# Performance work log

Measured on AMD Instinct MI355X. Metric: run time of the kernel, lower is better.

The kernel has to match this reference:

```python
import jax, jax.numpy as jnp
import numpy as np

EMB = 256
HEADS = 8
DH = EMB // HEADS
GRID = (64, 64)
WIN = (8, 8)
B = 16
L = GRID[0] * GRID[1]
LOG100 = float(np.log(100.0))
LN_EPS = 1e-5


def _build_shift_mask():
    # Standard Swin shifted-window attention mask (static, numpy).
    Hh, Ww = GRID; wh, ww = WIN
    sh, sw = wh // 2, ww // 2
    img = np.zeros((Hh, Ww), dtype=np.int32)
    cnt = 0
    for hs in (slice(0, -wh), slice(-wh, -sh), slice(-sh, None)):
        for ws in (slice(0, -ww), slice(-ww, -sw), slice(-sw, None)):
            img[hs, ws] = cnt; cnt += 1
    m = img.reshape(Hh // wh, wh, Ww // ww, ww).transpose(0, 2, 1, 3).reshape(-1, wh * ww)
    mask = np.where(m[:, None, :] != m[:, :, None], -1e4, 0.0).astype(np.float32)
    return jnp.asarray(mask)  # (nWin, N, N)

SHIFT_MASK = _build_shift_mask()


def _layernorm(x, w, b):
    mu = jnp.mean(x, axis=-1, keepdims=True)
    var = jnp.mean(jnp.square(x - mu), axis=-1, keepdims=True)
    return (x - mu) * jax.lax.rsqrt(var + LN_EPS) * w + b


def _window_cos_msa(x, qkv_w, qkv_b, proj_w, proj_b, logit_scale, shifted):
    # x: (B, L, C)
    Hh, Ww = GRID; wh, ww = WIN
    nH, nW = Hh // wh, Ww // ww
    N = wh * ww
    Bb, _, C = x.shape
    xg = x.reshape(Bb, Hh, Ww, C)
    if shifted:
        xg = jnp.roll(xg, (-(wh // 2), -(ww // 2)), axis=(1, 2))
    # window partition -> (B, nWin, N, C)
    xw = xg.reshape(Bb, nH, wh, nW, ww, C).transpose(0, 1, 3, 2, 4, 5).reshape(Bb, nH * nW, N, C)
    qkv = xw @ qkv_w + qkv_b                      # (B, nWin, N, 3C)
    qkv = qkv.reshape(Bb, nH * nW, N, 3, HEADS, DH).transpose(3, 0, 1, 4, 2, 5)
    q, k, v = qkv[0], qkv[1], qkv[2]              # (B, nWin, H, N, DH)
    qn = q / jnp.clip(jnp.linalg.norm(q, axis=-1, keepdims=True), 1e-6)
    kn = k / jnp.clip(jnp.linalg.norm(k, axis=-1, keepdims=True), 1e-6)
    scale = jnp.exp(jnp.minimum(logit_scale, LOG100)).reshape(1, 1, HEADS, 1, 1)
    attn = jnp.einsum('bwhnd,bwhmd->bwhnm', qn, kn) * scale  # cosine attention
    if shifted:
        attn = attn + SHIFT_MASK[None, :, None, :, :]
    attn = jax.nn.softmax(attn, axis=-1)
    out = jnp.einsum('bwhnm,bwhmd->bwhnd', attn, v)          # (B, nWin, H, N, DH)
    out = out.transpose(0, 1, 3, 2, 4).reshape(Bb, nH * nW, N, C)
    out = out @ proj_w + proj_b
    # window merge -> (B, H, W, C)
    out = out.reshape(Bb, nH, nW, wh, ww, C).transpose(0, 1, 3, 2, 4, 5).reshape(Bb, Hh, Ww, C)
    if shifted:
        out = jnp.roll(out, (wh // 2, ww // 2), axis=(1, 2))
    return out.reshape(Bb, Hh * Ww, C)


def _mlp(x, w1, b1, w2, b2):
    h = jax.nn.gelu(x @ w1 + b1, approximate=False)
    return h @ w2 + b2


def setup_inputs() -> dict:
    key = jax.random.key(0)
    ks = jax.random.split(key, 12)
    s = 0.02
    d = {}
    d['x'] = jax.random.normal(ks[0], (B, L, EMB), jnp.float32)
    for i, p in enumerate(('wmsa', 'swmsa')):
        d[p + '_qkv_w'] = jax.random.normal(ks[1 + 3 * i], (EMB, 3 * EMB), jnp.float32) * s
        d[p + '_qkv_b'] = jnp.zeros((3 * EMB,), jnp.float32)
        d[p + '_proj_w'] = jax.random.normal(ks[2 + 3 * i], (EMB, EMB), jnp.float32) * s
        d[p + '_proj_b'] = jnp.zeros((EMB,), jnp.float32)
        d[p + '_logit_scale'] = jnp.full((HEADS,), float(np.log(10.0)), jnp.float32)
    d['ln_w'] = jnp.ones((EMB,), jnp.float32)
    d['ln_b'] = jnp.zeros((EMB,), jnp.float32)
    d['mlp_w1'] = jax.random.normal(ks[7], (EMB, 4 * EMB), jnp.float32) * s
    d['mlp_b1'] = jnp.zeros((4 * EMB,), jnp.float32)
    d['mlp_w2'] = jax.random.normal(ks[8], (4 * EMB, EMB), jnp.float32) * s
    d['mlp_b2'] = jnp.zeros((EMB,), jnp.float32)
    return d


def reference(x, wmsa_qkv_w, wmsa_qkv_b, wmsa_proj_w, wmsa_proj_b, wmsa_logit_scale,
              swmsa_qkv_w, swmsa_qkv_b, swmsa_proj_w, swmsa_proj_b, swmsa_logit_scale,
              ln_w, ln_b, mlp_w1, mlp_b1, mlp_w2, mlp_b2):
    # x = x + LN(WMSA(x)); x = x + LN(MLP(x)); x = x + LN(SWMSA(x)); x = x + LN(MLP(x))
    x = x + _layernorm(_window_cos_msa(x, wmsa_qkv_w, wmsa_qkv_b, wmsa_proj_w, wmsa_proj_b, wmsa_logit_scale, False), ln_w, ln_b)
    x = x + _layernorm(_mlp(x, mlp_w1, mlp_b1, mlp_w2, mlp_b2), ln_w, ln_b)
    x = x + _layernorm(_window_cos_msa(x, swmsa_qkv_w, swmsa_qkv_b, swmsa_proj_w, swmsa_proj_b, swmsa_logit_scale, True), ln_w, ln_b)
    x = x + _layernorm(_mlp(x, mlp_w1, mlp_b1, mlp_w2, mlp_b2), ln_w, ln_b)
    return x
```

## Files before the change

### kernel.cpp

```cpp
#include <hip/hip_runtime.h>
#include <math.h>

typedef __attribute__((ext_vector_type(4))) float f32x4;
typedef __attribute__((ext_vector_type(8))) short bf16x8;

__device__ __forceinline__ short f2bf(float f) {
  unsigned u = __builtin_bit_cast(unsigned, f);
  u += 0x7FFFu + ((u >> 16) & 1u);
  return (short)(u >> 16);
}
__device__ __forceinline__ float bf2f(short s) {
  unsigned u = ((unsigned)(unsigned short)s) << 16;
  return __builtin_bit_cast(float, u);
}

#define MFMA(A, B, C) __builtin_amdgcn_mfma_f32_16x16x32_bf16((A), (B), (C), 0, 0, 0)

#define GLOAD16(gsrc, ldst)                                                      \
  __builtin_amdgcn_global_load_lds(                                              \
      (const __attribute__((address_space(1))) void*)(gsrc),                     \
      (__attribute__((address_space(3))) void*)(ldst), 16, 0, 0)

#define LOG100 4.605170185988092f

__global__ __launch_bounds__(256) void convert_kernel(
    const float* __restrict__ x,
    const float* __restrict__ qw0, const float* __restrict__ qw1,
    const float* __restrict__ pw0, const float* __restrict__ pw1,
    const float* __restrict__ w1, const float* __restrict__ w2,
    short* __restrict__ xb,
    short* __restrict__ qwT0, short* __restrict__ qwT1,
    short* __restrict__ pwT0, short* __restrict__ pwT1,
    short* __restrict__ w1T, short* __restrict__ w2T) {
  int bid = blockIdx.x;
  int tid = threadIdx.x;
  if (bid < 8192) {
    int base = (bid * 256 + tid) * 8;
    bf16x8 o;
#pragma unroll
    for (int j = 0; j < 8; ++j) o[j] = f2bf(x[base + j]);
    *(bf16x8*)&xb[base] = o;
    return;
  }
  int idx = (bid - 8192) * 256 + tid;
  if (idx < 196608) { int n = idx >> 8, k = idx & 255; qwT0[idx] = f2bf(qw0[k * 768 + n]); return; }
  idx -= 196608;
  if (idx < 196608) { int n = idx >> 8, k = idx & 255; qwT1[idx] = f2bf(qw1[k * 768 + n]); return; }
  idx -= 196608;
  if (idx < 65536) { int n = idx >> 8, k = idx & 255; pwT0[idx] = f2bf(pw0[k * 256 + n]); return; }
  idx -= 65536;
  if (idx < 65536) { int n = idx >> 8, k = idx & 255; pwT1[idx] = f2bf(pw1[k * 256 + n]); return; }
  idx -= 65536;
  if (idx < 262144) { int n = idx >> 8, k = idx & 255; w1T[idx] = f2bf(w1[k * 1024 + n]); return; }
  idx -= 262144;
  { int n = idx >> 10, k = idx & 1023; w2T[idx] = f2bf(w2[k * 256 + n]); }
}

template <bool SHIFTED>
__global__ __launch_bounds__(256) void qkv_kernel(
    const short* __restrict__ xb, const short* __restrict__ wT,
    const float* __restrict__ bias,
    short* __restrict__ Q, short* __restrict__ K, short* __restrict__ V,
    int mblk_base) {
  __shared__ short Alds[64][72];
  __shared__ short Blds[256][72];
  const int mloc = blockIdx.x;
  const int mg = mblk_base + mloc;
  const int which = blockIdx.y;
  const int b = mg >> 6, wi = mg & 63;
  const int h0 = (wi >> 3) << 3, w0c = (wi & 7) << 3;
  const int tid = threadIdx.x;
  const int lane = tid & 63, wid = tid >> 6;
  const int l15 = lane & 15, lg = lane >> 4;

  f32x4 zf = {0.f, 0.f, 0.f, 0.f};
  f32x4 acc[4][4];
#pragma unroll
  for (int i = 0; i < 4; ++i)
#pragma unroll
    for (int j = 0; j < 4; ++j) acc[i][j] = zf;

#pragma unroll 1
  for (int kc = 0; kc < 4; ++kc) {
    __syncthreads();
    {
      int c8 = (tid & 7) * 8;
#pragma unroll
      for (int it = 0; it < 2; ++it) {
        int r = (tid >> 3) + it * 32;
        int hs = h0 + (r >> 3), ws2 = w0c + (r & 7);
        if (SHIFTED) { hs = (hs + 4) & 63; ws2 = (ws2 + 4) & 63; }
        int t = b * 4096 + hs * 64 + ws2;
        *(bf16x8*)&Alds[r][c8] = *(const bf16x8*)&xb[t * 256 + kc * 64 + c8];
      }
    }
    {
      int k8 = (tid & 7) * 8;
      int cw = tid >> 3;
#pragma unroll
      for (int p = 0; p < 8; ++p) {
        int col = cw + p * 32;
        *(bf16x8*)&Blds[col][k8] = *(const bf16x8*)&wT[(which * 256 + col) * 256 + kc * 64 + k8];
      }
    }
    __syncthreads();
#pragma unroll
    for (int ks = 0; ks < 2; ++ks) {
      bf16x8 af[4], bfr[4];
#pragma unroll
      for (int ti = 0; ti < 4; ++ti) af[ti] = *(bf16x8*)&Alds[ti * 16 + l15][ks * 32 + lg * 8];
#pragma unroll
      for (int tj = 0; tj < 4; ++tj) bfr[tj] = *(bf16x8*)&Blds[wid * 64 + tj * 16 + l15][ks * 32 + lg * 8];
#pragma unroll
      for (int ti = 0; ti < 4; ++ti)
#pragma unroll
        for (int tj = 0; tj < 4; ++tj) acc[ti][tj] = MFMA(af[ti], bfr[tj], acc[ti][tj]);
    }
  }
  short* outp = (which == 0) ? Q : (which == 1) ? K : V;
#pragma unroll
  for (int tj = 0; tj < 4; ++tj) {
    int c = wid * 64 + tj * 16 + l15;
    int h = c >> 5, d = c & 31;
    float bv = bias[which * 256 + c];
    int hb = (mloc * 8 + h) * 2048;
#pragma unroll
    for (int ti = 0; ti < 4; ++ti) {
#pragma unroll
      for (int idx = 0; idx < 4; ++idx) {
        int n = ti * 16 + lg * 4 + idx;
        float v = acc[ti][tj][idx] + bv;
        int off = hb + (which == 2 ? (d * 64 + n) : (n * 32 + d));
        outp[off] = f2bf(v);
      }
    }
  }
}

template <bool SHIFTED>
__global__ __launch_bounds__(256) void attn_kernel(
    const short* __restrict__ Q, const short* __restrict__ K, const short* __restrict__ V,
    const float* __restrict__ logit_scale,
    const short* __restrict__ projT, const float* __restrict__ proj_b,
    const float* __restrict__ ln_w, const float* __restrict__ ln_b,
    const float* x_old, float* x_new, short* x_new_bf,
    int mblk_base) {
  __shared__ short Plds[4][64][72];
  __shared__ short Olds[64][264];
  __shared__ float red1[4][64], red2[4][64];
  __shared__ int ids[64];

  const int mloc = blockIdx.x;
  const int mg = mblk_base + mloc;
  const int b = mg >> 6, wi = mg & 63;
  const int h0 = (wi >> 3) << 3, w0c = (wi & 7) << 3;
  const int tid = threadIdx.x;
  const int lane = tid & 63, wid = tid >> 6;
  const int l15 = lane & 15, lg = lane >> 4;

  if (SHIFTED) {
    if (tid < 64) {
      int hs = h0 + (tid >> 3), ws2 = w0c + (tid & 7);
      int rr = (hs < 56) ? 0 : ((hs < 60) ? 1 : 2);
      int rc = (ws2 < 56) ? 0 : ((ws2 < 60) ? 1 : 2);
      ids[tid] = rr * 3 + rc;
    }
    __syncthreads();
  }

  f32x4 zf = {0.f, 0.f, 0.f, 0.f};

#pragma unroll 1
  for (int hp = 0; hp < 2; ++hp) {
    const int h = wid * 2 + hp;
    const short* Qh = Q + (mloc * 8 + h) * 2048;
    const short* Kh = K + (mloc * 8 + h) * 2048;
    const short* Vt = V + (mloc * 8 + h) * 2048;
    const float sc = __expf(fminf(logit_scale[h], LOG100));

    bf16x8 qf[4];
#pragma unroll
    for (int ti = 0; ti < 4; ++ti) {
      qf[ti] = *(const bf16x8*)&Qh[(ti * 16 + l15) * 32 + lg * 8];
      float ss = 0.f;
#pragma unroll
      for (int j = 0; j < 8; ++j) { float q = bf2f(qf[ti][j]); ss += q * q; }
      ss += __shfl_xor(ss, 16); ss += __shfl_xor(ss, 32);
      float f = sc / fmaxf(sqrtf(ss), 1e-6f);
#pragma unroll
      for (int j = 0; j < 8; ++j) qf[ti][j] = f2bf(bf2f(qf[ti][j]) * f);
    }
    bf16x8 kf[4];
#pragma unroll
    for (int tj = 0; tj < 4; ++tj) {
      kf[tj] = *(const bf16x8*)&Kh[(tj * 16 + l15) * 32 + lg * 8];
      float ss = 0.f;
#pragma unroll
      for (int j = 0; j < 8; ++j) { float k = bf2f(kf[tj][j]); ss += k * k; }
      ss += __shfl_xor(ss, 16); ss += __shfl_xor(ss, 32);
      float f = 1.f / fmaxf(sqrtf(ss), 1e-6f);
#pragma unroll
      for (int j = 0; j < 8; ++j) kf[tj][j] = f2bf(bf2f(kf[tj][j]) * f);
    }
    f32x4 sacc[4][4];
#pragma unroll
    for (int ti = 0; ti < 4; ++ti)
#pragma unroll
      for (int tj = 0; tj < 4; ++tj) sacc[ti][tj] = MFMA(qf[ti], kf[tj], zf);

    if (SHIFTED) {
      int idc[4];
#pragma unroll
      for (int tj = 0; tj < 4; ++tj) idc[tj] = ids[tj * 16 + l15];
#pragma unroll
      for (int ti = 0; ti < 4; ++ti)
#pragma unroll
        for (int idx = 0; idx < 4; ++idx) {
          int idr = ids[ti * 16 + lg * 4 + idx];
#pragma unroll
          for (int tj = 0; tj < 4; ++tj)
            if (idr != idc[tj]) sacc[ti][tj][idx] += -1e4f;
        }
    }
#pragma unroll
    for (int ti = 0; ti < 4; ++ti) {
#pragma unroll
      for (int idx = 0; idx < 4; ++idx) {
        float m = fmaxf(fmaxf(sacc[ti][0][idx], sacc[ti][1][idx]),
                        fmaxf(sacc[ti][2][idx], sacc[ti][3][idx]));
        m = fmaxf(m, __shfl_xor(m, 1));
        m = fmaxf(m, __shfl_xor(m, 2));
        m = fmaxf(m, __shfl_xor(m, 4));
        m = fmaxf(m, __shfl_xor(m, 8));
        float e0 = __expf(sacc[ti][0][idx] - m);
        float e1 = __expf(sacc[ti][1][idx] - m);
        float e2 = __expf(sacc[ti][2][idx] - m);
        float e3 = __expf(sacc[ti][3][idx] - m);
        float s = e0 + e1 + e2 + e3;
        s += __shfl_xor(s, 1); s += __shfl_xor(s, 2);
        s += __shfl_xor(s, 4); s += __shfl_xor(s, 8);
        float inv = 1.f / s;
        sacc[ti][0][idx] = e0 * inv; sacc[ti][1][idx] = e1 * inv;
        sacc[ti][2][idx] = e2 * inv; sacc[ti][3][idx] = e3 * inv;
      }
    }
#pragma unroll
    for (int ti = 0; ti < 4; ++ti)
#pragma unroll
      for (int tj = 0; tj < 4; ++tj)
#pragma unroll
        for (int idx = 0; idx < 4; ++idx)
          Plds[wid][ti * 16 + lg * 4 + idx][tj * 16 + l15] = f2bf(sacc[ti][tj][idx]);

    f32x4 oacc[4][2];
#pragma unroll
    for (int ti = 0; ti < 4; ++ti)
#pragma unroll
      for (int vj = 0; vj < 2; ++vj) oacc[ti][vj] = zf;
#pragma unroll
    for (int ks = 0; ks < 2; ++ks) {
      bf16x8 pf[4], vf[2];
#pragma unroll
      for (int ti = 0; ti < 4; ++ti) pf[ti] = *(bf16x8*)&Plds[wid][ti * 16 + l15][ks * 32 + lg * 8];
#pragma unroll
      for (int vj = 0; vj < 2; ++vj) vf[vj] = *(const bf16x8*)&Vt[(vj * 16 + l15) * 64 + ks * 32 + lg * 8];
#pragma unroll
      for (int ti = 0; ti < 4; ++ti)
#pragma unroll
        for (int vj = 0; vj < 2; ++vj) oacc[ti][vj] = MFMA(pf[ti], vf[vj], oacc[ti][vj]);
    }
#pragma unroll
    for (int ti = 0; ti < 4; ++ti)
#pragma unroll
      for (int vj = 0; vj < 2; ++vj)
#pragma unroll
        for (int idx = 0; idx < 4; ++idx)
          Olds[ti * 16 + lg * 4 + idx][h * 32 + vj * 16 + l15] = f2bf(oacc[ti][vj][idx]);
  }
  __syncthreads();

  f32x4 pacc[4][4];
#pragma unroll
  for (int i = 0; i < 4; ++i)
#pragma unroll
    for (int j = 0; j < 4; ++j) pacc[i][j] = zf;
#pragma unroll
  for (int kc = 0; kc < 8; ++kc) {
    bf16x8 af[4], bfr[4];
#pragma unroll
    for (int ti = 0; ti < 4; ++ti) af[ti] = *(bf16x8*)&Olds[ti * 16 + l15][kc * 32 + lg * 8];
#pragma unroll
    for (int tj = 0; tj < 4; ++tj)
      bfr[tj] = *(const bf16x8*)&projT[(wid * 64 + tj * 16 + l15) * 256 + kc * 32 + lg * 8];
#pragma unroll
    for (int ti = 0; ti < 4; ++ti)
#pragma unroll
      for (int tj = 0; tj < 4; ++tj) pacc[ti][tj] = MFMA(af[ti], bfr[tj], pacc[ti][tj]);
  }
#pragma unroll
  for (int tj = 0; tj < 4; ++tj) {
    float bv = proj_b[wid * 64 + tj * 16 + l15];
#pragma unroll
    for (int ti = 0; ti < 4; ++ti)
#pragma unroll
      for (int idx = 0; idx < 4; ++idx) pacc[ti][tj][idx] += bv;
  }

#pragma unroll
  for (int ti = 0; ti < 4; ++ti) {
#pragma unroll
    for (int idx = 0; idx < 4; ++idx) {
      float s1 = 0.f, s2 = 0.f;
#pragma unroll
      for (int tj = 0; tj < 4; ++tj) { float v = pacc[ti][tj][idx]; s1 += v; s2 += v * v; }
#pragma unroll
      for (int m = 1; m <= 8; m <<= 1) { s1 += __shfl_xor(s1, m); s2 += __shfl_xor(s2, m); }
      if (l15 == 0) { int row = ti * 16 + lg * 4 + idx; red1[wid][row] = s1; red2[wid][row] = s2; }
    }
  }
  __syncthreads();
#pragma unroll
  for (int ti = 0; ti < 4; ++ti) {
#pragma unroll
    for (int idx = 0; idx < 4; ++idx) {
      int row = ti * 16 + lg * 4 + idx;
      float t1 = red1[0][row] + red1[1][row] + red1[2][row] + red1[3][row];
      float t2 = red2[0][row] + red2[1][row] + red2[2][row] + red2[3][row];
      float mu = t1 * 0.00390625f;
      float var = t2 * 0.00390625f - mu * mu;
      float rstd = rsqrtf(var + 1e-5f);
      int hs = h0 + (row >> 3), ws2 = w0c + (row & 7);
      if (SHIFTED) { hs = (hs + 4) & 63; ws2 = (ws2 + 4) & 63; }
      int tok = b * 4096 + hs * 64 + ws2;
#pragma unroll
      for (int tj = 0; tj < 4; ++tj) {
        int c = wid * 64 + tj * 16 + l15;
        float yn = (pacc[ti][tj][idx] - mu) * rstd * ln_w[c] + ln_b[c];
        float xn = x_old[tok * 256 + c] + yn;
        x_new[tok * 256 + c] = xn;
        x_new_bf[tok * 256 + c] = f2bf(xn);
      }
    }
  }
}

__global__ __launch_bounds__(512) void mlp1_kernel(
    const short* __restrict__ xb,
    const short* __restrict__ w1T, const float* __restrict__ b1,
    short* __restrict__ hidden, int tok_base) {
  __shared__ short A[128 * 64];
  __shared__ short Bs[256 * 64];
  const int mloc = blockIdx.x;
  const int n0 = blockIdx.y * 256;
  const int tid = threadIdx.x;
  const int lane = tid & 63, wid = tid >> 6;
  const int wr = wid >> 2, wc = wid & 3;
  const int l15 = lane & 15, lg = lane >> 4;
  const int lrow = lane >> 3, lcol8 = (lane & 7) * 8;

  f32x4 zf = {0.f, 0.f, 0.f, 0.f};
  f32x4 acc[4][4];
#pragma unroll
  for (int i = 0; i < 4; ++i)
#pragma unroll
    for (int j = 0; j < 4; ++j) acc[i][j] = zf;

  const int tok0 = tok_base + mloc * 128;

#pragma unroll 1
  for (int kc = 0; kc < 4; ++kc) {
    __syncthreads();
#pragma unroll
    for (int it = 0; it < 2; ++it) {
      int r0 = wid * 16 + it * 8;
      GLOAD16(&xb[(size_t)(tok0 + r0 + lrow) * 256 + kc * 64 + lcol8], &A[r0 * 64]);
    }
#pragma unroll
    for (int it = 0; it < 4; ++it) {
      int c0 = wid * 32 + it * 8;
      GLOAD16(&w1T[(size_t)(n0 + c0 + lrow) * 256 + kc * 64 + lcol8], &Bs[c0 * 64]);
    }
    __syncthreads();
#pragma unroll
    for (int ks = 0; ks < 2; ++ks) {
      bf16x8 af[4], bfr[4];
#pragma unroll
      for (int ti = 0; ti < 4; ++ti)
        af[ti] = *(bf16x8*)&A[(wr * 64 + ti * 16 + l15) * 64 + ks * 32 + lg * 8];
#pragma unroll
      for (int tj = 0; tj < 4; ++tj)
        bfr[tj] = *(bf16x8*)&Bs[(wc * 64 + tj * 16 + l15) * 64 + ks * 32 + lg * 8];
#pragma unroll
      for (int ti = 0; ti < 4; ++ti)
#pragma unroll
        for (int tj = 0; tj < 4; ++tj) acc[ti][tj] = MFMA(af[ti], bfr[tj], acc[ti][tj]);
    }
  }
#pragma unroll
  for (int tj = 0; tj < 4; ++tj) {
    int col = n0 + wc * 64 + tj * 16 + l15;
    float bv = b1[col];
#pragma unroll
    for (int ti = 0; ti < 4; ++ti) {
      int rbase = mloc * 128 + wr * 64 + ti * 16 + lg * 4;
#pragma unroll
      for (int idx = 0; idx < 4; ++idx) {
        float v = acc[ti][tj][idx] + bv;
        float g = 0.5f * v * (1.f + erff(v * 0.70710678118654752f));
        hidden[(size_t)(rbase + idx) * 1024 + col] = f2bf(g);
      }
    }
  }
}

__global__ __launch_bounds__(512) void mlp2_kernel(
    const short* __restrict__ hidden,
    const short* __restrict__ w2T, const float* __restrict__ b2,
    const float* __restrict__ ln_w, const float* __restrict__ ln_b,
    const float* x_old, float* x_new, short* x_new_bf, int tok_base) {
  __shared__ short A[128 * 64];
  __shared__ short Bs[256 * 64];
  __shared__ float red1[128][4], red2[128][4];
  const int mloc = blockIdx.x;
  const int tid = threadIdx.x;
  const int lane = tid & 63, wid = tid >> 6;
  const int wr = wid >> 2, wc = wid & 3;
  const int l15 = lane & 15, lg = lane >> 4;
  const int lrow = lane >> 3, lcol8 = (lane & 7) * 8;

  f32x4 zf = {0.f, 0.f, 0.f, 0.f};
  f32x4 acc[4][4];
#pragma unroll
  for (int i = 0; i < 4; ++i)
#pragma unroll
    for (int j = 0; j < 4; ++j) acc[i][j] = zf;

#pragma unroll 1
  for (int kc = 0; kc < 16; ++kc) {
    __syncthreads();
#pragma unroll
    for (int it = 0; it < 2; ++it) {
      int r0 = wid * 16 + it * 8;
      GLOAD16(&hidden[(size_t)(mloc * 128 + r0 + lrow) * 1024 + kc * 64 + lcol8], &A[r0 * 64]);
    }
#pragma unroll
    for (int it = 0; it < 4; ++it) {
      int c0 = wid * 32 + it * 8;
      GLOAD16(&w2T[(size_t)(c0 + lrow) * 1024 + kc * 64 + lcol8], &Bs[c0 * 64]);
    }
    __syncthreads();
#pragma unroll
    for (int ks = 0; ks < 2; ++ks) {
      bf16x8 af[4], bfr[4];
#pragma unroll
      for (int ti = 0; ti < 4; ++ti)
        af[ti] = *(bf16x8*)&A[(wr * 64 + ti * 16 + l15) * 64 + ks * 32 + lg * 8];
#pragma unroll
      for (int tj = 0; tj < 4; ++tj)
        bfr[tj] = *(bf16x8*)&Bs[(wc * 64 + tj * 16 + l15) * 64 + ks * 32 + lg * 8];
#pragma unroll
      for (int ti = 0; ti < 4; ++ti)
#pragma unroll
        for (int tj = 0; tj < 4; ++tj) acc[ti][tj] = MFMA(af[ti], bfr[tj], acc[ti][tj]);
    }
  }
#pragma unroll
  for (int tj = 0; tj < 4; ++tj) {
    float bv = b2[wc * 64 + tj * 16 + l15];
#pragma unroll
    for (int ti = 0; ti < 4; ++ti)
#pragma unroll
      for (int idx = 0; idx < 4; ++idx) acc[ti][tj][idx] += bv;
  }
#pragma unroll
  for (int ti = 0; ti < 4; ++ti) {
#pragma unroll
    for (int idx = 0; idx < 4; ++idx) {
      float s1 = 0.f, s2 = 0.f;
#pragma unroll
      for (int tj = 0; tj < 4; ++tj) { float v = acc[ti][tj][idx]; s1 += v; s2 += v * v; }
#pragma unroll
      for (int m = 1; m <= 8; m <<= 1) { s1 += __shfl_xor(s1, m); s2 += __shfl_xor(s2, m); }
      if (l15 == 0) {
        int row = wr * 64 + ti * 16 + lg * 4 + idx;
        red1[row][wc] = s1; red2[row][wc] = s2;
      }
    }
  }
  __syncthreads();
#pragma unroll
  for (int ti = 0; ti < 4; ++ti) {
#pragma unroll
    for (int idx = 0; idx < 4; ++idx) {
      int row = wr * 64 + ti * 16 + lg * 4 + idx;
      float t1 = red1[row][0] + red1[row][1] + red1[row][2] + red1[row][3];
      float t2 = red2[row][0] + red2[row][1] + red2[row][2] + red2[row][3];
      float mu = t1 * 0.00390625f;
      float var = t2 * 0.00390625f - mu * mu;
      float rstd = rsqrtf(var + 1e-5f);
      size_t tok = (size_t)tok_base + mloc * 128 + row;
#pragma unroll
      for (int tj = 0; tj < 4; ++tj) {
        int c = wc * 64 + tj * 16 + l15;
        float yn = (acc[ti][tj][idx] - mu) * rstd * ln_w[c] + ln_b[c];
        float xn = x_old[tok * 256 + c] + yn;
        x_new[tok * 256 + c] = xn;
        x_new_bf[tok * 256 + c] = f2bf(xn);
      }
    }
  }
}

extern "C" void kernel_launch(void* const* d_in, const int* in_sizes, int n_in,
                              void* d_out, int out_size, void* d_ws, size_t ws_size,
                              hipStream_t stream) {
  (void)in_sizes; (void)n_in; (void)out_size;
  const float* x  = (const float*)d_in[0];
  const float* qw[2] = {(const float*)d_in[1], (const float*)d_in[6]};
  const float* qb[2] = {(const float*)d_in[2], (const float*)d_in[7]};
  const float* pw[2] = {(const float*)d_in[3], (const float*)d_in[8]};
  const float* pb[2] = {(const float*)d_in[4], (const float*)d_in[9]};
  const float* ls[2] = {(const float*)d_in[5], (const float*)d_in[10]};
  const float* lnw = (const float*)d_in[11];
  const float* lnb = (const float*)d_in[12];
  const float* w1 = (const float*)d_in[13];
  const float* b1 = (const float*)d_in[14];
  const float* w2 = (const float*)d_in[15];
  const float* b2 = (const float*)d_in[16];
  float* xout = (float*)d_out;

  char* ws = (char*)d_ws;
  short* xb = (short*)ws;

  int nchunk = 1;
  for (; nchunk < 16; nchunk *= 2) {
    size_t need = 33554432ull + (size_t)(1024 / nchunk) * 131072ull + 2097152ull;
    if (need <= ws_size) break;
  }
  int nmb = 1024 / nchunk;
  int nmlp = 512 / nchunk;
  char* region = ws + 33554432;
  short* Qb = (short*)region;
  short* Kb = (short*)(region + (size_t)nmb * 32768);
  short* Vb = (short*)(region + (size_t)nmb * 65536);
  short* hid = (short*)region;
  char* wbase = region + (size_t)nmb * 131072ull;
  short* qwT[2] = {(short*)wbase, (short*)(wbase + 393216)};
  short* pwT[2] = {(short*)(wbase + 786432), (short*)(wbase + 917504)};
  short* w1T = (short*)(wbase + 1048576);
  short* w2T = (short*)(wbase + 1572864);

  convert_kernel<<<12288, 256, 0, stream>>>(x, qw[0], qw[1], pw[0], pw[1], w1, w2,
                                            xb, qwT[0], qwT[1], pwT[0], pwT[1], w1T, w2T);
  for (int c = 0; c < nchunk; ++c) {
    qkv_kernel<false><<<dim3(nmb, 3), 256, 0, stream>>>(xb, qwT[0], qb[0], Qb, Kb, Vb, c * nmb);
    attn_kernel<false><<<nmb, 256, 0, stream>>>(Qb, Kb, Vb, ls[0], pwT[0], pb[0], lnw, lnb,
                                                x, xout, xb, c * nmb);
  }
  for (int c = 0; c < nchunk; ++c) {
    mlp1_kernel<<<dim3(nmlp, 4), 512, 0, stream>>>(xb, w1T, b1, hid, c * nmlp * 128);
    mlp2_kernel<<<nmlp, 512, 0, stream>>>(hid, w2T, b2, lnw, lnb, xout, xout, xb, c * nmlp * 128);
  }
  for (int c = 0; c < nchunk; ++c) {
    qkv_kernel<true><<<dim3(nmb, 3), 256, 0, stream>>>(xb, qwT[1], qb[1], Qb, Kb, Vb, c * nmb);
    attn_kernel<true><<<nmb, 256, 0, stream>>>(Qb, Kb, Vb, ls[1], pwT[1], pb[1], lnw, lnb,
                                               xout, xout, xb, c * nmb);
  }
  for (int c = 0; c < nchunk; ++c) {
    mlp1_kernel<<<dim3(nmlp, 4), 512, 0, stream>>>(xb, w1T, b1, hid, c * nmlp * 128);
    mlp2_kernel<<<nmlp, 512, 0, stream>>>(hid, w2T, b2, lnw, lnb, xout, xout, xb, c * nmlp * 128);
  }
}
```

Before: 978.1 us.

## Widen QKV GEMM to two windows per block with direct global-to-LDS loads

The QKV projection kernel now handles two windows (128 rows) per 512-thread block, so each weight tile staged in LDS is reused across twice as many tokens. Tiles are loaded with global_load_lds and the padded LDS layout is dropped, removing the register round-trip on loads. The attention kernel also gets a 2-blocks-per-CU occupancy hint, a fully unrolled head loop, and s_setprio raised around MFMA bursts. The trade-offs are possible LDS bank conflicts from the unpadded layout, more register pressure, and half as many QKV blocks.

```diff
diff --git a/kernel.cpp b/kernel.cpp
--- a/kernel.cpp
+++ b/kernel.cpp
@@ -57,21 +57,32 @@
 }
 
 template <bool SHIFTED>
-__global__ __launch_bounds__(256) void qkv_kernel(
+__global__ __launch_bounds__(512) void qkv_kernel(
     const short* __restrict__ xb, const short* __restrict__ wT,
     const float* __restrict__ bias,
     short* __restrict__ Q, short* __restrict__ K, short* __restrict__ V,
     int mblk_base) {
-  __shared__ short Alds[64][72];
-  __shared__ short Blds[256][72];
+  __shared__ short A[128 * 64];
+  __shared__ short Bs[256 * 64];
   const int mloc = blockIdx.x;
-  const int mg = mblk_base + mloc;
   const int which = blockIdx.y;
-  const int b = mg >> 6, wi = mg & 63;
-  const int h0 = (wi >> 3) << 3, w0c = (wi & 7) << 3;
   const int tid = threadIdx.x;
   const int lane = tid & 63, wid = tid >> 6;
+  const int wr = wid >> 2, wc = wid & 3;
   const int l15 = lane & 15, lg = lane >> 4;
+  const int lrow = lane >> 3, lcol8 = (lane & 7) * 8;
+
+  int tokA[2];
+#pragma unroll
+  for (int it = 0; it < 2; ++it) {
+    int r = wid * 16 + it * 8 + lrow;
+    int mg = mblk_base + mloc * 2 + (r >> 6);
+    int b = mg >> 6, wi = mg & 63;
+    int hs = ((wi >> 3) << 3) + ((r >> 3) & 7);
+    int ws2 = ((wi & 7) << 3) + (r & 7);
+    if (SHIFTED) { hs = (hs + 4) & 63; ws2 = (ws2 + 4) & 63; }
+    tokA[it] = b * 4096 + hs * 64 + ws2;
+  }
 
   f32x4 zf = {0.f, 0.f, 0.f, 0.f};
   f32x4 acc[4][4];
@@ -83,34 +94,26 @@
 #pragma unroll 1
   for (int kc = 0; kc < 4; ++kc) {
     __syncthreads();
-    {
-      int c8 = (tid & 7) * 8;
-#pragma unroll
-      for (int it = 0; it < 2; ++it) {
-        int r = (tid >> 3) + it * 32;
-        int hs = h0 + (r >> 3), ws2 = w0c + (r & 7);
-        if (SHIFTED) { hs = (hs + 4) & 63; ws2 = (ws2 + 4) & 63; }
-        int t = b * 4096 + hs * 64 + ws2;
-        *(bf16x8*)&Alds[r][c8] = *(const bf16x8*)&xb[t * 256 + kc * 64 + c8];
-      }
-    }
-    {
-      int k8 = (tid & 7) * 8;
-      int cw = tid >> 3;
-#pragma unroll
-      for (int p = 0; p < 8; ++p) {
-        int col = cw + p * 32;
-        *(bf16x8*)&Blds[col][k8] = *(const bf16x8*)&wT[(which * 256 + col) * 256 + kc * 64 + k8];
-      }
+#pragma unroll
+    for (int it = 0; it < 2; ++it) {
+      int r0 = wid * 16 + it * 8;
+      GLOAD16(&xb[(size_t)tokA[it] * 256 + kc * 64 + lcol8], &A[r0 * 64]);
+    }
+#pragma unroll
+    for (int it = 0; it < 4; ++it) {
+      int c0 = wid * 32 + it * 8;
+      GLOAD16(&wT[(size_t)(which * 256 + c0 + lrow) * 256 + kc * 64 + lcol8], &Bs[c0 * 64]);
     }
     __syncthreads();
 #pragma unroll
     for (int ks = 0; ks < 2; ++ks) {
       bf16x8 af[4], bfr[4];
 #pragma unroll
-      for (int ti = 0; ti < 4; ++ti) af[ti] = *(bf16x8*)&Alds[ti * 16 + l15][ks * 32 + lg * 8];
-#pragma unroll
-      for (int tj = 0; tj < 4; ++tj) bfr[tj] = *(bf16x8*)&Blds[wid * 64 + tj * 16 + l15][ks * 32 + lg * 8];
+      for (int ti = 0; ti < 4; ++ti)
+        af[ti] = *(bf16x8*)&A[(wr * 64 + ti * 16 + l15) * 64 + ks * 32 + lg * 8];
+#pragma unroll
+      for (int tj = 0; tj < 4; ++tj)
+        bfr[tj] = *(bf16x8*)&Bs[(wc * 64 + tj * 16 + l15) * 64 + ks * 32 + lg * 8];
 #pragma unroll
       for (int ti = 0; ti < 4; ++ti)
 #pragma unroll
@@ -118,12 +121,13 @@
     }
   }
   short* outp = (which == 0) ? Q : (which == 1) ? K : V;
+  const int lw = mloc * 2 + wr;
 #pragma unroll
   for (int tj = 0; tj < 4; ++tj) {
-    int c = wid * 64 + tj * 16 + l15;
+    int c = wc * 64 + tj * 16 + l15;
     int h = c >> 5, d = c & 31;
     float bv = bias[which * 256 + c];
-    int hb = (mloc * 8 + h) * 2048;
+    int hb = (lw * 8 + h) * 2048;
 #pragma unroll
     for (int ti = 0; ti < 4; ++ti) {
 #pragma unroll
@@ -138,7 +142,7 @@
 }
 
 template <bool SHIFTED>
-__global__ __launch_bounds__(256) void attn_kernel(
+__global__ __launch_bounds__(256, 2) void attn_kernel(
     const short* __restrict__ Q, const short* __restrict__ K, const short* __restrict__ V,
     const float* __restrict__ logit_scale,
     const short* __restrict__ projT, const float* __restrict__ proj_b,
@@ -170,7 +174,7 @@
 
   f32x4 zf = {0.f, 0.f, 0.f, 0.f};
 
-#pragma unroll 1
+#pragma unroll
   for (int hp = 0; hp < 2; ++hp) {
     const int h = wid * 2 + hp;
     const short* Qh = Q + (mloc * 8 + h) * 2048;
@@ -203,10 +207,12 @@
       for (int j = 0; j < 8; ++j) kf[tj][j] = f2bf(bf2f(kf[tj][j]) * f);
     }
     f32x4 sacc[4][4];
+    __builtin_amdgcn_s_setprio(1);
 #pragma unroll
     for (int ti = 0; ti < 4; ++ti)
 #pragma unroll
       for (int tj = 0; tj < 4; ++tj) sacc[ti][tj] = MFMA(qf[ti], kf[tj], zf);
+    __builtin_amdgcn_s_setprio(0);
 
     if (SHIFTED) {
       int idc[4];
@@ -264,10 +270,12 @@
       for (int ti = 0; ti < 4; ++ti) pf[ti] = *(bf16x8*)&Plds[wid][ti * 16 + l15][ks * 32 + lg * 8];
 #pragma unroll
       for (int vj = 0; vj < 2; ++vj) vf[vj] = *(const bf16x8*)&Vt[(vj * 16 + l15) * 64 + ks * 32 + lg * 8];
+      __builtin_amdgcn_s_setprio(1);
 #pragma unroll
       for (int ti = 0; ti < 4; ++ti)
 #pragma unroll
         for (int vj = 0; vj < 2; ++vj) oacc[ti][vj] = MFMA(pf[ti], vf[vj], oacc[ti][vj]);
+      __builtin_amdgcn_s_setprio(0);
     }
 #pragma unroll
     for (int ti = 0; ti < 4; ++ti)
@@ -292,10 +300,12 @@
 #pragma unroll
     for (int tj = 0; tj < 4; ++tj)
       bfr[tj] = *(const bf16x8*)&projT[(wid * 64 + tj * 16 + l15) * 256 + kc * 32 + lg * 8];
+    __builtin_amdgcn_s_setprio(1);
 #pragma unroll
     for (int ti = 0; ti < 4; ++ti)
 #pragma unroll
       for (int tj = 0; tj < 4; ++tj) pacc[ti][tj] = MFMA(af[ti], bfr[tj], pacc[ti][tj]);
+    __builtin_amdgcn_s_setprio(0);
   }
 #pragma unroll
   for (int tj = 0; tj < 4; ++tj) {
@@ -553,7 +563,7 @@
   convert_kernel<<<12288, 256, 0, stream>>>(x, qw[0], qw[1], pw[0], pw[1], w1, w2,
                                             xb, qwT[0], qwT[1], pwT[0], pwT[1], w1T, w2T);
   for (int c = 0; c < nchunk; ++c) {
-    qkv_kernel<false><<<dim3(nmb, 3), 256, 0, stream>>>(xb, qwT[0], qb[0], Qb, Kb, Vb, c * nmb);
+    qkv_kernel<false><<<dim3(nmb / 2, 3), 512, 0, stream>>>(xb, qwT[0], qb[0], Qb, Kb, Vb, c * nmb);
     attn_kernel<false><<<nmb, 256, 0, stream>>>(Qb, Kb, Vb, ls[0], pwT[0], pb[0], lnw, lnb,
                                                 x, xout, xb, c * nmb);
   }
@@ -562,7 +572,7 @@
     mlp2_kernel<<<nmlp, 512, 0, stream>>>(hid, w2T, b2, lnw, lnb, xout, xout, xb, c * nmlp * 128);
   }
   for (int c = 0; c < nchunk; ++c) {
-    qkv_kernel<true><<<dim3(nmb, 3), 256, 0, stream>>>(xb, qwT[1], qb[1], Qb, Kb, Vb, c * nmb);
+    qkv_kernel<true><<<dim3(nmb / 2, 3), 512, 0, stream>>>(xb, qwT[1], qb[1], Qb, Kb, Vb, c * nmb);
     attn_kernel<true><<<nmb, 256, 0, stream>>>(Qb, Kb, Vb, ls[1], pwT[1], pb[1], lnw, lnb,
                                                xout, xout, xb, c * nmb);
   }
```

After: 1.070 ms. 1.09x slower.
